# Kernel optimization log

Measured on AMD Instinct MI355X. Metric: run time of the kernel, lower is better.

The kernel has to match this reference:

```python
import jax, jax.numpy as jnp
import numpy as np
from jax import lax

B, L, N = 64, 1024, 64
IN_SZ, MEM_SZ, DEC = 128, 1024, 3


def setup_inputs() -> dict:
    key = jax.random.key(0)
    ks = jax.random.split(key, 8)
    x = jax.random.normal(ks[0], (B, L, N), dtype=jnp.float32)
    # sensor net: Linear(N -> IN_SZ) with bias (stored as [in, out])
    W_sense = jax.random.normal(ks[1], (N, IN_SZ), dtype=jnp.float32) / np.sqrt(N)
    b_sense = jax.random.normal(ks[2], (IN_SZ,), dtype=jnp.float32) * 0.01
    # nBRC: ff_im Linear(IN_SZ -> 3*MEM_SZ, bias=False), ff_mm Linear(MEM_SZ -> 2*MEM_SZ, bias=False)
    W_im = jax.random.normal(ks[3], (IN_SZ, 3 * MEM_SZ), dtype=jnp.float32) / np.sqrt(IN_SZ)
    W_mm = jax.random.normal(ks[4], (MEM_SZ, 2 * MEM_SZ), dtype=jnp.float32) / np.sqrt(MEM_SZ)
    # actor net: Linear(MEM_SZ -> DEC) with bias
    W_act = jax.random.normal(ks[5], (MEM_SZ, DEC), dtype=jnp.float32) / np.sqrt(MEM_SZ)
    b_act = jax.random.normal(ks[6], (DEC,), dtype=jnp.float32) * 0.01
    return {"x": x, "W_sense": W_sense, "b_sense": b_sense,
            "W_im": W_im, "W_mm": W_mm, "W_act": W_act, "b_act": b_act}


def reference(x, W_sense, b_sense, W_im, W_mm, W_act, b_act):
    # sense: applied per-token (flattened in torch; equivalent broadcasted matmul)
    inputs = x @ W_sense + b_sense                      # [B, L, IN_SZ]
    # precompute the input projection for all timesteps in one GEMM
    proj = inputs @ W_im                                 # [B, L, 3*MEM_SZ]
    proj_t = jnp.moveaxis(proj, 1, 0)                    # [L, B, 3*MEM_SZ]
    h0 = jnp.zeros((x.shape[0], MEM_SZ), dtype=x.dtype)

    def step(h, p):
        i_a, i_c, i_o = jnp.split(p, 3, axis=-1)         # each [B, MEM_SZ]
        m = h @ W_mm                                      # [B, 2*MEM_SZ]
        m_a, m_c = jnp.split(m, 2, axis=-1)
        a = 1.0 + jnp.tanh(i_a + m_a)
        c = jax.nn.sigmoid(i_c + m_c)
        hn = c * h + (1.0 - c) * jnp.tanh(i_o + a * h)
        return hn, hn

    _, hs = lax.scan(step, h0, proj_t)                    # [L, B, MEM_SZ]
    memory = jnp.moveaxis(hs, 0, 1)                       # [B, L, MEM_SZ]
    logits = memory @ W_act + b_act                       # [B, L, DEC]
    return jax.nn.softmax(logits, axis=-1)
```

## Files before the change

### kernel.cpp

```cpp
#include <hip/hip_runtime.h>
#include <hip/hip_bf16.h>


#define B_TOT 64
#define L_SEQ 1024
#define N_IN 64
#define INSZ 128
#define MEM 1024
#define DEC 3

#define NGROUP 8
#define BG 8
#define NMEM 32
#define RING 16

typedef __hip_bfloat16 bf16;
typedef short bf16x8 __attribute__((ext_vector_type(8)));
typedef float f32x4 __attribute__((ext_vector_type(4)));
typedef int i32x4 __attribute__((ext_vector_type(4)));
typedef unsigned long long ull;

#define OFF_INPUTS 0
#define SZ_INPUTS  (L_SEQ * 64 * INSZ * 2)
#define OFF_WMM    (OFF_INPUTS + SZ_INPUTS)
#define SZ_WMM     (128 * 32 * 64 * 8 * 2)
#define OFF_WIM    (OFF_WMM + SZ_WMM)
#define SZ_WIM     (192 * 4 * 64 * 8 * 2)
#define OFF_HBUF   (OFF_WIM + SZ_WIM)
#define SZ_HBUF    (RING * NGROUP * BG * MEM * 2)
#define OFF_CTR    (OFF_HBUF + SZ_HBUF)
#define SZ_CTR     ((8192 + 256) * 4)

__device__ __forceinline__ float fast_tanh(float x) {
    float e = __expf(2.f * x);
    return 1.f - 2.f / (e + 1.f);
}
__device__ __forceinline__ float fast_sigmoid(float x) {
    return 1.f / (1.f + __expf(-x));
}

__global__ void k_sense(const float* __restrict__ x, const float* __restrict__ Ws,
                        const float* __restrict__ bs, bf16* __restrict__ inputs) {
    int t = blockIdx.x;
    int tid = threadIdx.x;
    __shared__ float xls[64][64];
    __shared__ float wls[64][128];
    for (int idx = tid; idx < 64 * 64; idx += 256) {
        int b = idx >> 6, k = idx & 63;
        xls[b][k] = x[((size_t)b * L_SEQ + t) * N_IN + k];
    }
    for (int idx = tid; idx < 64 * 128; idx += 256) {
        int k = idx >> 7, j = idx & 127;
        wls[k][j] = Ws[k * INSZ + j];
    }
    __syncthreads();
    int j = tid & 127;
    int bh = tid >> 7;
    float bj = bs[j];
    for (int bi = 0; bi < 32; ++bi) {
        int b = bh * 32 + bi;
        float acc = bj;
#pragma unroll
        for (int k = 0; k < 64; ++k) acc += xls[b][k] * wls[k][j];
        inputs[((size_t)t * 64 + b) * INSZ + j] = (bf16)acc;
    }
}

__global__ void k_pack(const float* __restrict__ Wmm, const float* __restrict__ Wim,
                       bf16* __restrict__ pmm, bf16* __restrict__ pim) {
    int idx = blockIdx.x * 256 + threadIdx.x;
    const int NMMF = 128 * 32 * 64 * 8;
    if (idx < NMMF) {
        int j = idx & 7, lane = (idx >> 3) & 63, kb = (idx >> 9) & 31, ct = idx >> 14;
        int n = ct * 16 + (lane & 15);
        int k = kb * 32 + ((lane >> 4) << 3) + j;
        pmm[idx] = (bf16)Wmm[(size_t)k * 2048 + n];
    } else {
        int idx2 = idx - NMMF;
        if (idx2 < 192 * 4 * 64 * 8) {
            int j = idx2 & 7, lane = (idx2 >> 3) & 63, kb = (idx2 >> 9) & 3, ct = idx2 >> 11;
            int n = ct * 16 + (lane & 15);
            int k = kb * 32 + ((lane >> 4) << 3) + j;
            pim[idx2] = (bf16)Wim[(size_t)k * 3072 + n];
        }
    }
}

__launch_bounds__(256, 1)
__global__ void k_main(const bf16* __restrict__ inputs, const bf16* __restrict__ pmm,
                       const bf16* __restrict__ pim, const float* __restrict__ Wact,
                       const float* __restrict__ bact, bf16* __restrict__ hbuf,
                       float* __restrict__ out, unsigned int* __restrict__ ctr) {
    const int g = blockIdx.x & 7;
    const int m = blockIdx.x >> 3;
    const int tid = (int)threadIdx.x;
    const int wave = tid >> 6;
    const int lane = tid & 63;
    const int r16 = lane & 15;
    const int q = lane >> 4;
    const int col = tid & 31;
    const int p = col >> 4;
    const int cl = col & 15;
    const int bloc = tid >> 5;

    __shared__ bf16 Hlds[16][1032];
    __shared__ float ilds[2][3][2][8][16];
    __shared__ float mlds[4][8][16];
    __shared__ float ownh[8][32];
    __shared__ bf16 hstage[8][32];
    __shared__ float wact_lds[3072];
    __shared__ float aplds[4][3];
    __shared__ float bactl[3];
    __shared__ unsigned idsl[256];
    __shared__ int fflagl;
    __shared__ float outbuf[L_SEQ * 3];

    for (int idx = tid; idx < 16 * 1032; idx += 256) ((bf16*)Hlds)[idx] = (bf16)0.f;
    for (int idx = tid; idx < 3072; idx += 256) wact_lds[idx] = Wact[idx];
    if (tid < 3) bactl[tid] = bact[tid];

    bf16x8 wb[32];
    {
        int ct = (wave >> 1) * 64 + m * 2 + (wave & 1);
#pragma unroll
        for (int kb = 0; kb < 32; ++kb)
            wb[kb] = *(const bf16x8*)(pmm + (((size_t)ct * 32 + kb) * 64 + lane) * 8);
    }
    bf16x8 wi[2][4];
    if (wave < 3) {
#pragma unroll
        for (int tl = 0; tl < 2; ++tl) {
            int ct2 = wave * 64 + m * 2 + tl;
#pragma unroll
            for (int kb2 = 0; kb2 < 4; ++kb2)
                wi[tl][kb2] = *(const bf16x8*)(pim + (((size_t)ct2 * 4 + kb2) * 64 + lane) * 8);
        }
    }
    ownh[bloc][col] = 0.f;

    unsigned int* flags   = ctr + g * 512;
    unsigned int* flagsL2 = ctr + 4096 + g * 512;
    unsigned int* ids     = ctr + 8192;

    unsigned xid;
    asm volatile("s_getreg_b32 %0, hwreg(HW_REG_XCC_ID)" : "=s"(xid));
    if (tid == 0)
        __hip_atomic_store(&ids[g * 32 + m], xid + 1u, __ATOMIC_RELAXED,
                           __HIP_MEMORY_SCOPE_AGENT);
    if (wave == 0) {
        int sb = 1 << 20;
        unsigned v0 = 0, v1 = 0, v2 = 0, v3 = 0;
        bool all = false;
        while (!all && --sb > 0) {
            v0 = __hip_atomic_load(&ids[lane], __ATOMIC_RELAXED, __HIP_MEMORY_SCOPE_AGENT);
            v1 = __hip_atomic_load(&ids[64 + lane], __ATOMIC_RELAXED, __HIP_MEMORY_SCOPE_AGENT);
            v2 = __hip_atomic_load(&ids[128 + lane], __ATOMIC_RELAXED, __HIP_MEMORY_SCOPE_AGENT);
            v3 = __hip_atomic_load(&ids[192 + lane], __ATOMIC_RELAXED, __HIP_MEMORY_SCOPE_AGENT);
            all = (bool)__all((int)(v0 && v1 && v2 && v3));
        }
        idsl[lane] = v0; idsl[64 + lane] = v1; idsl[128 + lane] = v2; idsl[192 + lane] = v3;
    }
    __syncthreads();
    if (tid == 0) {
        int f = 1;
        for (int g2 = 0; g2 < 8; ++g2) {
            unsigned r = idsl[g2 * 32];
            for (int k2 = 1; k2 < 32; ++k2) f &= (idsl[g2 * 32 + k2] == r);
        }
        fflagl = f;
    }
    __syncthreads();
    const bool fastf = (fflagl != 0);

    struct I2 { f32x4 a0, a1; };
    auto comp_iacc = [&](int t) -> I2 {
        I2 r;
        r.a0 = (f32x4){0.f, 0.f, 0.f, 0.f};
        r.a1 = (f32x4){0.f, 0.f, 0.f, 0.f};
        if (wave < 3) {
            int brow = g * 8 + (r16 & 7);
#pragma unroll
            for (int kb2 = 0; kb2 < 4; ++kb2) {
                bf16x8 af = *(const bf16x8*)(inputs +
                    ((size_t)t * 64 + brow) * INSZ + kb2 * 32 + q * 8);
                r.a0 = __builtin_amdgcn_mfma_f32_16x16x32_bf16(af, wi[0][kb2], r.a0, 0, 0, 0);
                r.a1 = __builtin_amdgcn_mfma_f32_16x16x32_bf16(af, wi[1][kb2], r.a1, 0, 0, 0);
            }
        }
        return r;
    };

    auto actor_emit = [&](int hrow) {
        float p0 = 0.f, p1 = 0.f, p2 = 0.f;
        int c0 = tid * 4;
        const bf16* hp = &Hlds[hrow][c0];
#pragma unroll
        for (int i = 0; i < 4; ++i) {
            float hv = (float)hp[i];
            p0 += hv * wact_lds[(c0 + i) * 3 + 0];
            p1 += hv * wact_lds[(c0 + i) * 3 + 1];
            p2 += hv * wact_lds[(c0 + i) * 3 + 2];
        }
#pragma unroll
        for (int off = 32; off >= 1; off >>= 1) {
            p0 += __shfl_xor(p0, off);
            p1 += __shfl_xor(p1, off);
            p2 += __shfl_xor(p2, off);
        }
        if (lane == 0) { aplds[wave][0] = p0; aplds[wave][1] = p1; aplds[wave][2] = p2; }
    };
    auto actor_fin = [&](int tout) {
        float l0 = aplds[0][0] + aplds[1][0] + aplds[2][0] + aplds[3][0] + bactl[0];
        float l1 = aplds[0][1] + aplds[1][1] + aplds[2][1] + aplds[3][1] + bactl[1];
        float l2 = aplds[0][2] + aplds[1][2] + aplds[2][2] + aplds[3][2] + bactl[2];
        float mx = fmaxf(l0, fmaxf(l1, l2));
        float e0 = __expf(l0 - mx), e1 = __expf(l1 - mx), e2 = __expf(l2 - mx);
        float inv = 1.f / (e0 + e1 + e2);
        outbuf[tout * 3 + 0] = e0 * inv;
        outbuf[tout * 3 + 1] = e1 * inv;
        outbuf[tout * 3 + 2] = e2 * inv;
    };

    I2 iacc = comp_iacc(0);

#pragma clang loop unroll(disable)
    for (int t = 0; t < L_SEQ; ++t) {
        if (t != 0 && (t & (RING - 1)) == 0)
            __builtin_amdgcn_fence(__ATOMIC_ACQUIRE, "agent");

        if (wave < 3 && q < 2) {
#pragma unroll
            for (int reg = 0; reg < 4; ++reg) {
                ilds[t & 1][wave][0][q * 4 + reg][r16] = iacc.a0[reg];
                ilds[t & 1][wave][1][q * 4 + reg][r16] = iacc.a1[reg];
            }
        }
        {
            const bf16* src = hbuf +
                ((size_t)(((t + RING - 1) & (RING - 1)) * NGROUP + g)) * BG * MEM;
            int f0 = tid, f1 = 256 + tid, f2 = 512 + tid, f3 = 768 + tid;
            i32x4 a0 = *(const i32x4*)(src + (f0 >> 7) * MEM + (f0 & 127) * 8);
            i32x4 a1 = *(const i32x4*)(src + (f1 >> 7) * MEM + (f1 & 127) * 8);
            i32x4 a2 = *(const i32x4*)(src + (f2 >> 7) * MEM + (f2 & 127) * 8);
            i32x4 a3 = *(const i32x4*)(src + (f3 >> 7) * MEM + (f3 & 127) * 8);
            *(i32x4*)(&Hlds[f0 >> 7][(f0 & 127) * 8]) = a0;
            *(i32x4*)(&Hlds[f1 >> 7][(f1 & 127) * 8]) = a1;
            *(i32x4*)(&Hlds[f2 >> 7][(f2 & 127) * 8]) = a2;
            *(i32x4*)(&Hlds[f3 >> 7][(f3 & 127) * 8]) = a3;
        }
        __syncthreads();

        {
            f32x4 m0 = {0.f, 0.f, 0.f, 0.f};
            f32x4 m1 = {0.f, 0.f, 0.f, 0.f};
#pragma unroll
            for (int i = 0; i < 16; ++i) {
                bf16x8 a0 = *(const bf16x8*)(&Hlds[r16][(2 * i) * 32 + q * 8]);
                bf16x8 a1 = *(const bf16x8*)(&Hlds[r16][(2 * i + 1) * 32 + q * 8]);
                m0 = __builtin_amdgcn_mfma_f32_16x16x32_bf16(a0, wb[2 * i], m0, 0, 0, 0);
                m1 = __builtin_amdgcn_mfma_f32_16x16x32_bf16(a1, wb[2 * i + 1], m1, 0, 0, 0);
            }
            if (q < 2) {
#pragma unroll
                for (int reg = 0; reg < 4; ++reg)
                    mlds[wave][q * 4 + reg][r16] = m0[reg] + m1[reg];
            }
        }
        if (m < 8 && t > 0) actor_emit(m);
        __syncthreads();

        {
            float ma = mlds[p][bloc][cl];
            float mc = mlds[2 + p][bloc][cl];
            float ia = ilds[t & 1][0][p][bloc][cl];
            float ic = ilds[t & 1][1][p][bloc][cl];
            float io = ilds[t & 1][2][p][bloc][cl];
            float h0 = ownh[bloc][col];
            float a = 1.f + fast_tanh(ia + ma);
            float c = fast_sigmoid(ic + mc);
            float hn = c * h0 + (1.f - c) * fast_tanh(io + a * h0);
            ownh[bloc][col] = hn;
            hstage[bloc][col] = (bf16)hn;
        }
        __syncthreads();

        if (m < 8 && t > 0 && tid == 64) actor_fin(t - 1);

        if (tid < 64) {
            bf16* base = hbuf + ((size_t)((t & (RING - 1)) * NGROUP + g)) * BG * MEM;
            int row = lane >> 3, c = lane & 7;
            ull v = *(const ull*)(&hstage[row][c * 4]);
            ull* dst = (ull*)(base + (size_t)row * MEM + m * 32) + c;
            if (fastf) {
                *dst = v;
            } else {
                __hip_atomic_store(dst, v, __ATOMIC_RELAXED, __HIP_MEMORY_SCOPE_AGENT);
            }
            asm volatile("s_waitcnt vmcnt(0)" ::: "memory");
            if (lane == 0) {
                if (fastf) flagsL2[m * 16] = (unsigned)(t + 1);
                __hip_atomic_store(&flags[m * 16], (unsigned)(t + 1), __ATOMIC_RELAXED,
                                   __HIP_MEMORY_SCOPE_AGENT);
            }
        }

        if (t + 1 < L_SEQ) iacc = comp_iacc(t + 1);
        if (wave == 3) {
            unsigned target = (unsigned)(t + 1);
            unsigned vbest = (lane < 32) ? 0u : target;
            bool done = false;
            int rounds = 0;
            int sb = 1 << 20;
            while (!done && --sb > 0) {
                if (fastf && lane < 32 && vbest < target) {
                    const unsigned* a = flagsL2 + lane * 16;
                    unsigned vl;
                    asm volatile("global_load_dword %0, %1, off sc0\n\t"
                                 "s_waitcnt vmcnt(0)"
                                 : "=&v"(vl) : "v"(a) : "memory");
                    if (vl > vbest) vbest = vl;
                }
                if (lane < 32 && vbest < target && (!fastf || rounds >= 2)) {
                    unsigned vm = __hip_atomic_load(&flags[lane * 16], __ATOMIC_RELAXED,
                                                    __HIP_MEMORY_SCOPE_AGENT);
                    if (vm > vbest) vbest = vm;
                }
                done = (bool)__all((int)(vbest >= target));
                ++rounds;
                if (!done && rounds > 8) __builtin_amdgcn_s_sleep(1);
            }
        }
        __syncthreads();
    }

    if (m < 8) {
        __builtin_amdgcn_fence(__ATOMIC_ACQUIRE, "agent");
        const bf16* src = hbuf + ((size_t)(((L_SEQ - 1) & (RING - 1)) * NGROUP + g)) * BG * MEM +
                          (size_t)m * MEM;
        if (tid < 128) {
            *(i32x4*)(&Hlds[0][tid * 8]) = *(const i32x4*)(src + tid * 8);
        }
        __syncthreads();
        actor_emit(0);
        __syncthreads();
        if (tid == 0) actor_fin(L_SEQ - 1);
        __syncthreads();
        float* obase = out + (size_t)(g * 8 + m) * L_SEQ * 3;
        for (int idx = tid; idx < L_SEQ * 3; idx += 256)
            obase[idx] = outbuf[idx];
    }
}

extern "C" void kernel_launch(void* const* d_in, const int* in_sizes, int n_in,
                              void* d_out, int out_size, void* d_ws, size_t ws_size,
                              hipStream_t stream) {
    const float* x    = (const float*)d_in[0];
    const float* Ws   = (const float*)d_in[1];
    const float* bs   = (const float*)d_in[2];
    const float* Wim  = (const float*)d_in[3];
    const float* Wmm  = (const float*)d_in[4];
    const float* Wact = (const float*)d_in[5];
    const float* bact = (const float*)d_in[6];

    char* ws = (char*)d_ws;
    bf16* inputs = (bf16*)(ws + OFF_INPUTS);
    bf16* pmm    = (bf16*)(ws + OFF_WMM);
    bf16* pim    = (bf16*)(ws + OFF_WIM);
    bf16* hbuf   = (bf16*)(ws + OFF_HBUF);
    unsigned int* ctr = (unsigned int*)(ws + OFF_CTR);

    hipMemsetAsync(hbuf, 0, SZ_HBUF, stream);
    hipMemsetAsync(ctr, 0, SZ_CTR, stream);

    k_sense<<<L_SEQ, 256, 0, stream>>>(x, Ws, bs, inputs);
    k_pack<<<(128 * 32 * 64 * 8 + 192 * 4 * 64 * 8) / 256, 256, 0, stream>>>(Wmm, Wim, pmm, pim);
    k_main<<<NGROUP * NMEM, 256, 0, stream>>>(inputs, pmm, pim, Wact, bact, hbuf,
                                              (float*)d_out, ctr);
}
```

Baseline: 3.264 ms.

## Split recurrent matmul K across waves and poll per-wave flags directly

Each wave now covers a K-slice of the h@W_mm product for all four output tiles, loading its bf16 A fragments straight from the global ring buffer instead of staging the whole hidden state in LDS. Partial sums are reduced through a new LDS array. hbuf gets a new layout where each block's 32 columns are contiguous. Each wave polls only the flags of the 8 producer blocks it depends on, replacing the single wave-3 poll plus barrier at the end of each step. This is meant to cut the LDS staging copy and a block-wide barrier from the serial critical path. The actor softmax is delayed one more step, and hidden state is kept in a register rather than in LDS.

```diff
diff --git a/kernel.cpp b/kernel.cpp
--- a/kernel.cpp
+++ b/kernel.cpp
@@ -103,10 +103,8 @@
     const int cl = col & 15;
     const int bloc = tid >> 5;
 
-    __shared__ bf16 Hlds[16][1032];
     __shared__ float ilds[2][3][2][8][16];
-    __shared__ float mlds[4][8][16];
-    __shared__ float ownh[8][32];
+    __shared__ float mpart[4][4][8][16];
     __shared__ bf16 hstage[8][32];
     __shared__ float wact_lds[3072];
     __shared__ float aplds[4][3];
@@ -115,16 +113,18 @@
     __shared__ int fflagl;
     __shared__ float outbuf[L_SEQ * 3];
 
-    for (int idx = tid; idx < 16 * 1032; idx += 256) ((bf16*)Hlds)[idx] = (bf16)0.f;
     for (int idx = tid; idx < 3072; idx += 256) wact_lds[idx] = Wact[idx];
     if (tid < 3) bactl[tid] = bact[tid];
 
-    bf16x8 wb[32];
+    bf16x8 wb[4][8];
     {
-        int ct = (wave >> 1) * 64 + m * 2 + (wave & 1);
-#pragma unroll
-        for (int kb = 0; kb < 32; ++kb)
-            wb[kb] = *(const bf16x8*)(pmm + (((size_t)ct * 32 + kb) * 64 + lane) * 8);
+        int base_ct[4] = {2 * m, 2 * m + 1, 64 + 2 * m, 65 + 2 * m};
+#pragma unroll
+        for (int t4 = 0; t4 < 4; ++t4)
+#pragma unroll
+            for (int kk = 0; kk < 8; ++kk)
+                wb[t4][kk] = *(const bf16x8*)(pmm +
+                    (((size_t)base_ct[t4] * 32 + (wave * 8 + kk)) * 64 + lane) * 8);
     }
     bf16x8 wi[2][4];
     if (wave < 3) {
@@ -136,7 +136,7 @@
                 wi[tl][kb2] = *(const bf16x8*)(pim + (((size_t)ct2 * 4 + kb2) * 64 + lane) * 8);
         }
     }
-    ownh[bloc][col] = 0.f;
+    float hreg = 0.f;
 
     unsigned int* flags   = ctr + g * 512;
     unsigned int* flagsL2 = ctr + 4096 + g * 512;
@@ -190,17 +190,48 @@
         return r;
     };
 
-    auto actor_emit = [&](int hrow) {
-        float p0 = 0.f, p1 = 0.f, p2 = 0.f;
+    auto poll_own = [&](unsigned target) {
+        int k = wave * 8 + (lane & 7);
+        bool act = lane < 8;
+        unsigned vbest = act ? 0u : target;
+        bool done = false;
+        int rounds = 0;
+        int sb = 1 << 20;
+        while (!done && --sb > 0) {
+            if (fastf && act && vbest < target) {
+                const unsigned* a = flagsL2 + k * 16;
+                unsigned vl;
+                asm volatile("global_load_dword %0, %1, off sc0\n\t"
+                             "s_waitcnt vmcnt(0)"
+                             : "=&v"(vl) : "v"(a) : "memory");
+                if (vl > vbest) vbest = vl;
+            }
+            if (act && vbest < target && (!fastf || rounds >= 2)) {
+                unsigned vm = __hip_atomic_load(&flags[k * 16], __ATOMIC_RELAXED,
+                                                __HIP_MEMORY_SCOPE_AGENT);
+                if (vm > vbest) vbest = vm;
+            }
+            done = (bool)__all((int)(vbest >= target));
+            ++rounds;
+            if (!done && rounds > 8) __builtin_amdgcn_s_sleep(1);
+        }
+    };
+
+    auto actor_emit = [&](int t_src) {
         int c0 = tid * 4;
-        const bf16* hp = &Hlds[hrow][c0];
-#pragma unroll
-        for (int i = 0; i < 4; ++i) {
-            float hv = (float)hp[i];
-            p0 += hv * wact_lds[(c0 + i) * 3 + 0];
-            p1 += hv * wact_lds[(c0 + i) * 3 + 1];
-            p2 += hv * wact_lds[(c0 + i) * 3 + 2];
-        }
+        const bf16* hp = hbuf +
+            ((size_t)(((t_src & (RING - 1)) * NGROUP + g)) * (BG * MEM)) +
+            (c0 >> 5) * 256 + m * 32 + (c0 & 31);
+        ushort4 hv = *(const ushort4*)hp;
+        float h0 = __uint_as_float((unsigned)hv.x << 16);
+        float h1 = __uint_as_float((unsigned)hv.y << 16);
+        float h2 = __uint_as_float((unsigned)hv.z << 16);
+        float h3 = __uint_as_float((unsigned)hv.w << 16);
+        const f32x4* wp = (const f32x4*)&wact_lds[c0 * 3];
+        f32x4 w0 = wp[0], w1 = wp[1], w2 = wp[2];
+        float p0 = h0 * w0[0] + h1 * w0[3] + h2 * w1[2] + h3 * w2[1];
+        float p1 = h0 * w0[1] + h1 * w1[0] + h2 * w1[3] + h3 * w2[2];
+        float p2 = h0 * w0[2] + h1 * w1[1] + h2 * w2[0] + h3 * w2[3];
 #pragma unroll
         for (int off = 32; off >= 1; off >>= 1) {
             p0 += __shfl_xor(p0, off);
@@ -235,62 +266,64 @@
                 ilds[t & 1][wave][1][q * 4 + reg][r16] = iacc.a1[reg];
             }
         }
+
+        if (t > 0) poll_own((unsigned)t);
+
         {
-            const bf16* src = hbuf +
-                ((size_t)(((t + RING - 1) & (RING - 1)) * NGROUP + g)) * BG * MEM;
-            int f0 = tid, f1 = 256 + tid, f2 = 512 + tid, f3 = 768 + tid;
-            i32x4 a0 = *(const i32x4*)(src + (f0 >> 7) * MEM + (f0 & 127) * 8);
-            i32x4 a1 = *(const i32x4*)(src + (f1 >> 7) * MEM + (f1 & 127) * 8);
-            i32x4 a2 = *(const i32x4*)(src + (f2 >> 7) * MEM + (f2 & 127) * 8);
-            i32x4 a3 = *(const i32x4*)(src + (f3 >> 7) * MEM + (f3 & 127) * 8);
-            *(i32x4*)(&Hlds[f0 >> 7][(f0 & 127) * 8]) = a0;
-            *(i32x4*)(&Hlds[f1 >> 7][(f1 & 127) * 8]) = a1;
-            *(i32x4*)(&Hlds[f2 >> 7][(f2 & 127) * 8]) = a2;
-            *(i32x4*)(&Hlds[f3 >> 7][(f3 & 127) * 8]) = a3;
-        }
-        __syncthreads();
+            const bf16* lp = hbuf +
+                ((size_t)((((t - 1) & (RING - 1)) * NGROUP + g)) * (BG * MEM)) +
+                (size_t)(wave * 8) * 256 + ((r16 & 7) * 32 + q * 8);
+            bf16x8 af[8];
+#pragma unroll
+            for (int kk = 0; kk < 8; ++kk)
+                af[kk] = *(const bf16x8*)(lp + kk * 256);
+            f32x4 acc0 = {0.f, 0.f, 0.f, 0.f};
+            f32x4 acc1 = {0.f, 0.f, 0.f, 0.f};
+            f32x4 acc2 = {0.f, 0.f, 0.f, 0.f};
+            f32x4 acc3 = {0.f, 0.f, 0.f, 0.f};
+#pragma unroll
+            for (int kk = 0; kk < 8; ++kk) {
+                acc0 = __builtin_amdgcn_mfma_f32_16x16x32_bf16(af[kk], wb[0][kk], acc0, 0, 0, 0);
+                acc1 = __builtin_amdgcn_mfma_f32_16x16x32_bf16(af[kk], wb[1][kk], acc1, 0, 0, 0);
+                acc2 = __builtin_amdgcn_mfma_f32_16x16x32_bf16(af[kk], wb[2][kk], acc2, 0, 0, 0);
+                acc3 = __builtin_amdgcn_mfma_f32_16x16x32_bf16(af[kk], wb[3][kk], acc3, 0, 0, 0);
+            }
+            if (q < 2) {
+#pragma unroll
+                for (int reg = 0; reg < 4; ++reg) {
+                    mpart[wave][0][q * 4 + reg][r16] = acc0[reg];
+                    mpart[wave][1][q * 4 + reg][r16] = acc1[reg];
+                    mpart[wave][2][q * 4 + reg][r16] = acc2[reg];
+                    mpart[wave][3][q * 4 + reg][r16] = acc3[reg];
+                }
+            }
+        }
+        __syncthreads();
+
+        if (m < 8 && t >= 2 && tid == 64) actor_fin(t - 2);
 
         {
-            f32x4 m0 = {0.f, 0.f, 0.f, 0.f};
-            f32x4 m1 = {0.f, 0.f, 0.f, 0.f};
-#pragma unroll
-            for (int i = 0; i < 16; ++i) {
-                bf16x8 a0 = *(const bf16x8*)(&Hlds[r16][(2 * i) * 32 + q * 8]);
-                bf16x8 a1 = *(const bf16x8*)(&Hlds[r16][(2 * i + 1) * 32 + q * 8]);
-                m0 = __builtin_amdgcn_mfma_f32_16x16x32_bf16(a0, wb[2 * i], m0, 0, 0, 0);
-                m1 = __builtin_amdgcn_mfma_f32_16x16x32_bf16(a1, wb[2 * i + 1], m1, 0, 0, 0);
-            }
-            if (q < 2) {
-#pragma unroll
-                for (int reg = 0; reg < 4; ++reg)
-                    mlds[wave][q * 4 + reg][r16] = m0[reg] + m1[reg];
-            }
-        }
-        if (m < 8 && t > 0) actor_emit(m);
-        __syncthreads();
-
-        {
-            float ma = mlds[p][bloc][cl];
-            float mc = mlds[2 + p][bloc][cl];
+            float ma = mpart[0][p][bloc][cl] + mpart[1][p][bloc][cl]
+                     + mpart[2][p][bloc][cl] + mpart[3][p][bloc][cl];
+            float mc = mpart[0][2 + p][bloc][cl] + mpart[1][2 + p][bloc][cl]
+                     + mpart[2][2 + p][bloc][cl] + mpart[3][2 + p][bloc][cl];
             float ia = ilds[t & 1][0][p][bloc][cl];
             float ic = ilds[t & 1][1][p][bloc][cl];
             float io = ilds[t & 1][2][p][bloc][cl];
-            float h0 = ownh[bloc][col];
             float a = 1.f + fast_tanh(ia + ma);
             float c = fast_sigmoid(ic + mc);
-            float hn = c * h0 + (1.f - c) * fast_tanh(io + a * h0);
-            ownh[bloc][col] = hn;
+            float hn = c * hreg + (1.f - c) * fast_tanh(io + a * hreg);
+            hreg = hn;
             hstage[bloc][col] = (bf16)hn;
         }
         __syncthreads();
 
-        if (m < 8 && t > 0 && tid == 64) actor_fin(t - 1);
-
-        if (tid < 64) {
-            bf16* base = hbuf + ((size_t)((t & (RING - 1)) * NGROUP + g)) * BG * MEM;
+        if (wave == 3) {
+            bf16* base = hbuf +
+                ((size_t)(((t & (RING - 1)) * NGROUP + g)) * (BG * MEM)) + m * 256;
             int row = lane >> 3, c = lane & 7;
             ull v = *(const ull*)(&hstage[row][c * 4]);
-            ull* dst = (ull*)(base + (size_t)row * MEM + m * 32) + c;
+            ull* dst = (ull*)base + lane;
             if (fastf) {
                 *dst = v;
             } else {
@@ -303,45 +336,17 @@
                                    __HIP_MEMORY_SCOPE_AGENT);
             }
         }
-
         if (t + 1 < L_SEQ) iacc = comp_iacc(t + 1);
-        if (wave == 3) {
-            unsigned target = (unsigned)(t + 1);
-            unsigned vbest = (lane < 32) ? 0u : target;
-            bool done = false;
-            int rounds = 0;
-            int sb = 1 << 20;
-            while (!done && --sb > 0) {
-                if (fastf && lane < 32 && vbest < target) {
-                    const unsigned* a = flagsL2 + lane * 16;
-                    unsigned vl;
-                    asm volatile("global_load_dword %0, %1, off sc0\n\t"
-                                 "s_waitcnt vmcnt(0)"
-                                 : "=&v"(vl) : "v"(a) : "memory");
-                    if (vl > vbest) vbest = vl;
-                }
-                if (lane < 32 && vbest < target && (!fastf || rounds >= 2)) {
-                    unsigned vm = __hip_atomic_load(&flags[lane * 16], __ATOMIC_RELAXED,
-                                                    __HIP_MEMORY_SCOPE_AGENT);
-                    if (vm > vbest) vbest = vm;
-                }
-                done = (bool)__all((int)(vbest >= target));
-                ++rounds;
-                if (!done && rounds > 8) __builtin_amdgcn_s_sleep(1);
-            }
-        }
-        __syncthreads();
+        if (m < 8 && t > 0) actor_emit(t - 1);
     }
 
     if (m < 8) {
+        __syncthreads();
+        if (tid == 0) actor_fin(L_SEQ - 2);
+        poll_own((unsigned)L_SEQ);
         __builtin_amdgcn_fence(__ATOMIC_ACQUIRE, "agent");
-        const bf16* src = hbuf + ((size_t)(((L_SEQ - 1) & (RING - 1)) * NGROUP + g)) * BG * MEM +
-                          (size_t)m * MEM;
-        if (tid < 128) {
-            *(i32x4*)(&Hlds[0][tid * 8]) = *(const i32x4*)(src + tid * 8);
-        }
-        __syncthreads();
-        actor_emit(0);
+        __syncthreads();
+        actor_emit(L_SEQ - 1);
         __syncthreads();
         if (tid == 0) actor_fin(L_SEQ - 1);
         __syncthreads();
```

New measurement: 3.322 ms. About the same (+1.8%).
